# Performance work log

Measured on AMD Instinct MI355X. Metric: run time of the kernel, lower is better.

The kernel has to match this reference:

```python
import jax, jax.numpy as jnp
import numpy as np

N = 100000
E = 1_600_000
DIN = 24
DH = 64
DOUT = 12
NEG_SLOPE = 0.01  # torch F.leaky_relu default


def setup_inputs() -> dict:
    key = jax.random.key(0)
    ks = jax.random.split(key, 18)
    inp = {}
    inp["feats"] = jax.random.normal(ks[0], (N, DIN), dtype=jnp.float32)
    inp["e_w"] = jax.random.uniform(ks[1], (E, 1), dtype=jnp.float32)
    inp["snorm_n"] = jnp.ones((N, 1), dtype=jnp.float32)
    inp["snorm_e"] = jnp.ones((E, 1), dtype=jnp.float32)
    inp["src"] = jax.random.randint(ks[2], (E,), 0, N, dtype=jnp.int32)
    inp["dst"] = jax.random.randint(ks[3], (E,), 0, N, dtype=jnp.int32)
    s = 0.05
    inp["emb_h_W"] = jax.random.normal(ks[4], (DH, DIN), dtype=jnp.float32) * s
    inp["emb_h_b"] = jnp.zeros((DH,), dtype=jnp.float32)
    inp["emb_e_W"] = jax.random.normal(ks[5], (DH, 1), dtype=jnp.float32) * s
    inp["emb_e_b"] = jnp.zeros((DH,), dtype=jnp.float32)
    inp["W_self1"] = jax.random.normal(ks[6], (DH, DH), dtype=jnp.float32) * s
    inp["W_func1"] = jax.random.normal(ks[7], (DH, DH), dtype=jnp.float32) * s
    inp["attn1"] = jax.random.normal(ks[8], (3 * DH,), dtype=jnp.float32) * s
    inp["W_self2"] = jax.random.normal(ks[9], (DH, DH), dtype=jnp.float32) * s
    inp["W_func2"] = jax.random.normal(ks[10], (DH, DH), dtype=jnp.float32) * s
    inp["attn2"] = jax.random.normal(ks[11], (3 * DH,), dtype=jnp.float32) * s
    inp["lin1_W"] = jax.random.normal(ks[12], (DOUT, DH), dtype=jnp.float32) * s
    inp["lin1_b"] = jnp.zeros((DOUT,), dtype=jnp.float32)
    return inp


def _gat_layer(h, w_edge, src, dst, W_self, W_func, attn):
    # h: [N, d], w_edge: [E, d] edge embedding, attn: [3d]
    h_s = h @ W_self.T                       # linear_self(h)
    z = h @ W_func.T                         # linear_func(h)
    d = z.shape[-1]
    a_src, a_dst, a_w = attn[:d], attn[d:2 * d], attn[2 * d:]
    # attention score: W_a . [z_src, z_dst, w]  (decomposed to avoid [E,3d] concat)
    s_node_src = z @ a_src                   # [N]
    s_node_dst = z @ a_dst                   # [N]
    e = s_node_src[src] + s_node_dst[dst] + w_edge @ a_w  # [E]
    e = jax.nn.leaky_relu(e, NEG_SLOPE)
    # segment softmax over incoming edges per destination node
    m = jax.ops.segment_max(e, dst, num_segments=h.shape[0])
    ex = jnp.exp(e - m[dst])
    denom = jax.ops.segment_sum(ex, dst, num_segments=h.shape[0])
    alpha = ex / denom[dst]                  # [E]
    msg = alpha[:, None] * z[src]            # [E, d]
    agg = jax.ops.segment_sum(msg, dst, num_segments=h.shape[0])  # [N, d]
    # DGL: nodes with no incoming edges keep their old 'h' (not h_s + agg)
    in_deg = jax.ops.segment_sum(jnp.ones_like(e), dst, num_segments=h.shape[0])
    h_mid = jnp.where((in_deg > 0)[:, None], h_s + agg, h)
    return h + jax.nn.relu(h_mid)            # relu then residual


def reference(feats, e_w, snorm_n, snorm_e, src, dst,
              emb_h_W, emb_h_b, emb_e_W, emb_e_b,
              W_self1, W_func1, attn1, W_self2, W_func2, attn2,
              lin1_W, lin1_b):
    feats = feats.reshape(feats.shape[0], -1)
    h = feats @ emb_h_W.T + emb_h_b          # [N, DH]
    e = e_w @ emb_e_W.T + emb_e_b            # [E, DH]
    h = _gat_layer(h, e, src, dst, W_self1, W_func1, attn1)
    h = _gat_layer(h, e, src, dst, W_self2, W_func2, attn2)
    y = h @ lin1_W.T + lin1_b                # [N, DOUT]
    return y
```

## Files before the change

kernel.cpp:

```cpp
#include <hip/hip_runtime.h>
#include <hip/hip_fp16.h>

#define N_NODES 100000
#define N_EDGES 1600000
#define DIN 24
#define DH 64
#define DOUT 12
#define NEG_SLOPE 0.01f
#define NG 64
#define EPG (N_EDGES / NG)
#define NS 7
#define SLICE_N 16384
#define NTOT (NG * N_NODES)
#define SCAN_BLK 4096
#define LDSW 72

#define NB_HIST (NS * NG)
#define NB_SUMDEG ((N_NODES + 255) / 256)
#define NB_SCAN1N ((N_NODES + SCAN_BLK - 1) / SCAN_BLK)
#define NB_SCAT ((N_EDGES + 255) / 256)
#define NB_NODE ((N_NODES + 63) / 64)
#define NB_NODE_T ((NB_NODE + 1) / 2)
#define NB_AGG ((N_NODES + 7) / 8)

typedef _Float16 half8_t __attribute__((ext_vector_type(8)));
typedef float floatx4 __attribute__((ext_vector_type(4)));

__device__ __forceinline__ void dev_consts(const float* emb_e_W, const float* emb_e_b,
                                           const float* attn1, const float* attn2,
                                           float* consts) {
    int lane = threadIdx.x;
    if (lane >= 64) return;
    float w = emb_e_W[lane], b = emb_e_b[lane];
    float a1 = attn1[2 * DH + lane], a2 = attn2[2 * DH + lane];
    float c11 = w * a1, c01 = b * a1, c12 = w * a2, c02 = b * a2;
    for (int off = 32; off; off >>= 1) {
        c11 += __shfl_down(c11, off);
        c01 += __shfl_down(c01, off);
        c12 += __shfl_down(c12, off);
        c02 += __shfl_down(c02, off);
    }
    if (lane == 0) {
        consts[0] = c11; consts[1] = c01; consts[2] = c12; consts[3] = c02;
    }
}

__device__ __forceinline__ void dev_hist(int bid, const int* dst,
                                         unsigned char* deg, unsigned char* rank) {
    __shared__ unsigned cnt[SLICE_N / 4];
    int s = bid % NS, c = bid / NS;
    for (int i = threadIdx.x; i < SLICE_N / 4; i += 1024) cnt[i] = 0;
    __syncthreads();
    int nbase = s * SLICE_N;
    int start = c * EPG, end = start + EPG;
    for (int i = start + threadIdx.x; i < end; i += 1024) {
        int local = dst[i] - nbase;
        if ((unsigned)local < SLICE_N) {
            unsigned sh = (unsigned)(local & 3) * 8u;
            unsigned old = atomicAdd(&cnt[local >> 2], 1u << sh);
            rank[i] = (unsigned char)((old >> sh) & 255u);
        }
    }
    __syncthreads();
    int nmax = N_NODES - nbase;
    if (nmax > SLICE_N) nmax = SLICE_N;
    unsigned* dw = (unsigned*)(deg + (size_t)c * N_NODES + nbase);
    for (int l = threadIdx.x; l < (nmax >> 2); l += 1024) dw[l] = cnt[l];
}

__device__ __forceinline__ void dev_scan1(int bid, const int* in, int* out,
                                          int* part, int n) {
    __shared__ int lds[256];
    int t = threadIdx.x;
    int base = bid * SCAN_BLK + t * 16;
    int v[16];
    int s = 0;
#pragma unroll
    for (int i = 0; i < 16; ++i) {
        int idx = base + i;
        v[i] = (idx < n) ? in[idx] : 0;
        s += v[i];
    }
    lds[t] = s;
    __syncthreads();
    for (int off = 1; off < 256; off <<= 1) {
        int y = (t >= off) ? lds[t - off] : 0;
        __syncthreads();
        lds[t] += y;
        __syncthreads();
    }
    int run = lds[t] - s;
#pragma unroll
    for (int i = 0; i < 16; ++i) {
        int idx = base + i;
        if (idx < n) out[idx] = run;
        run += v[i];
    }
    if (t == 255) part[bid] = lds[255];
}

__device__ __forceinline__ void dev_scan2(int* part, int nblk, int* row_offN) {
    __shared__ int lds2[256];
    int t = threadIdx.x;
    int v[4];
    int s = 0;
#pragma unroll
    for (int i = 0; i < 4; ++i) {
        int idx = t * 4 + i;
        v[i] = (idx < nblk) ? part[idx] : 0;
        s += v[i];
    }
    lds2[t] = s;
    __syncthreads();
    for (int off = 1; off < 256; off <<= 1) {
        int y = (t >= off) ? lds2[t - off] : 0;
        __syncthreads();
        lds2[t] += y;
        __syncthreads();
    }
    int run = lds2[t] - s;
#pragma unroll
    for (int i = 0; i < 4; ++i) {
        int idx = t * 4 + i;
        if (idx < nblk) part[idx] = run;
        run += v[i];
    }
    if (row_offN) {
        __syncthreads();
        if (t == 0) row_offN[N_NODES] = N_EDGES - part[N_NODES >> 12];
    }
}

__device__ __forceinline__ void dev_sumdeg(int bid, const unsigned char* degB,
                                           int* degN, unsigned char* chunkOff) {
    int n = bid * 256 + threadIdx.x;
    if (n >= N_NODES) return;
    int run = 0;
    for (int g = 0; g < NG; ++g) {
        size_t idx = (size_t)g * N_NODES + n;
        int v = (int)degB[idx];
        chunkOff[idx] = (unsigned char)run;
        run += v;
    }
    degN[n] = run;
}

__device__ __forceinline__ void dev_nodeME(int bid, int stride,
                                           const float* feats, const float* embW,
                                           const float* embB,
                                           const float* Wself, const float* Wfunc,
                                           const float* attn,
                                           __half* h16, __half* zh, __half* hs16,
                                           float* s_src, float* s_dst) {
    __shared__ _Float16 lds[2 * 64 * LDSW];
    __shared__ _Float16 wembH[64 * 40];
    __shared__ float biasS[64];
    __shared__ _Float16 hbufH[4][16 * 72];
    int tid = threadIdx.x;
    for (int idx = tid; idx < 2 * 64 * 64; idx += 256) {
        int mat = idx >> 12, rem = idx & 4095;
        int o = rem >> 6, k = rem & 63;
        float v = mat ? Wfunc[rem] : Wself[rem];
        lds[(mat * 64 + o) * LDSW + k] = (_Float16)v;
    }
    for (int idx = tid; idx < 64 * 32; idx += 256) {
        int o = idx >> 5, k = idx & 31;
        wembH[o * 40 + k] = (_Float16)((k < DIN) ? embW[o * DIN + k] : 0.f);
    }
    if (tid < 64) biasS[tid] = embB[tid];
    __syncthreads();

    int wave = tid >> 6, lane = tid & 63;
    int quad = lane >> 4, lm = lane & 15;
    float asv[4], adv[4];
#pragma unroll
    for (int t = 0; t < 4; ++t) {
        asv[t] = attn[t * 16 + lm];
        adv[t] = attn[DH + t * 16 + lm];
    }
    const _Float16* bS = lds;
    const _Float16* bF = lds + 64 * LDSW;
    _Float16* hb = hbufH[wave];

    for (int tb = bid; tb < NB_NODE; tb += stride) {
        int n0 = (tb * 4 + wave) * 16;
        if (n0 >= N_NODES) continue;

        half8_t afE;
#pragma unroll
        for (int j = 0; j < 8; ++j) afE[j] = (_Float16)0.f;
        if (quad < 3) {
            const float* f = feats + (size_t)(n0 + lm) * DIN + quad * 8;
            float4 q0 = *(const float4*)(f);
            float4 q1 = *(const float4*)(f + 4);
            afE[0] = (_Float16)q0.x; afE[1] = (_Float16)q0.y;
            afE[2] = (_Float16)q0.z; afE[3] = (_Float16)q0.w;
            afE[4] = (_Float16)q1.x; afE[5] = (_Float16)q1.y;
            afE[6] = (_Float16)q1.z; afE[7] = (_Float16)q1.w;
        }
        floatx4 accE[4];
#pragma unroll
        for (int t = 0; t < 4; ++t) accE[t] = (floatx4)0.f;
#pragma unroll
        for (int t = 0; t < 4; ++t) {
            int o = t * 16 + lm;
            half8_t bE = *(const half8_t*)(wembH + o * 40 + quad * 8);
            accE[t] = __builtin_amdgcn_mfma_f32_16x16x32_f16(afE, bE, accE[t], 0, 0, 0);
        }
#pragma unroll
        for (int t = 0; t < 4; ++t) {
            float bv = biasS[t * 16 + lm];
#pragma unroll
            for (int r = 0; r < 4; ++r) {
                float hv = accE[t][r] + bv;
                int node = n0 + quad * 4 + r;
                h16[(size_t)node * DH + t * 16 + lm] = __float2half(hv);
                hb[(quad * 4 + r) * 72 + t * 16 + lm] = (_Float16)hv;
            }
        }
        half8_t afrag[2];
#pragma unroll
        for (int ks = 0; ks < 2; ++ks)
            afrag[ks] = *(const half8_t*)(hb + lm * 72 + ks * 32 + quad * 8);

        floatx4 accS[4], accF[4];
#pragma unroll
        for (int t = 0; t < 4; ++t) { accS[t] = (floatx4)0.f; accF[t] = (floatx4)0.f; }
#pragma unroll
        for (int t = 0; t < 4; ++t) {
            int o = t * 16 + lm;
#pragma unroll
            for (int ks = 0; ks < 2; ++ks) {
                int hoff = o * LDSW + ks * 32 + quad * 8;
                half8_t b1 = *(const half8_t*)(bS + hoff);
                half8_t b2 = *(const half8_t*)(bF + hoff);
                accS[t] = __builtin_amdgcn_mfma_f32_16x16x32_f16(afrag[ks], b1, accS[t], 0, 0, 0);
                accF[t] = __builtin_amdgcn_mfma_f32_16x16x32_f16(afrag[ks], b2, accF[t], 0, 0, 0);
            }
        }

        float ps[4] = {0.f, 0.f, 0.f, 0.f}, pd[4] = {0.f, 0.f, 0.f, 0.f};
#pragma unroll
        for (int t = 0; t < 4; ++t) {
#pragma unroll
            for (int r = 0; r < 4; ++r) {
                int node = n0 + quad * 4 + r;
                float zv = accF[t][r];
                zh[(size_t)node * DH + t * 16 + lm] = __float2half(zv);
                hs16[(size_t)node * DH + t * 16 + lm] = __float2half(accS[t][r]);
                ps[r] += zv * asv[t];
                pd[r] += zv * adv[t];
            }
        }
#pragma unroll
        for (int r = 0; r < 4; ++r) {
            float p1 = ps[r], p2 = pd[r];
            for (int off = 8; off; off >>= 1) {
                p1 += __shfl_xor(p1, off);
                p2 += __shfl_xor(p2, off);
            }
            if (lm == 0) {
                s_src[n0 + quad * 4 + r] = p1;
                s_dst[n0 + quad * 4 + r] = p2;
            }
        }
    }
}

__device__ __forceinline__ void dev_nodeM(int bid, int stride, const __half* h16,
                                          const float* Wself, const float* Wfunc,
                                          const float* attn,
                                          __half* zh, __half* hs16,
                                          float* s_src, float* s_dst) {
    __shared__ _Float16 lds[2 * 64 * LDSW];
    int tid = threadIdx.x;
    for (int idx = tid; idx < 2 * 64 * 64; idx += 256) {
        int mat = idx >> 12, rem = idx & 4095;
        int o = rem >> 6, k = rem & 63;
        float v = mat ? Wfunc[rem] : Wself[rem];
        lds[(mat * 64 + o) * LDSW + k] = (_Float16)v;
    }
    __syncthreads();

    int wave = tid >> 6, lane = tid & 63;
    int quad = lane >> 4, lm = lane & 15;
    float asv[4], adv[4];
#pragma unroll
    for (int t = 0; t < 4; ++t) {
        asv[t] = attn[t * 16 + lm];
        adv[t] = attn[DH + t * 16 + lm];
    }
    const _Float16* bS = lds;
    const _Float16* bF = lds + 64 * LDSW;

    for (int tb = bid; tb < NB_NODE; tb += stride) {
        int n0 = (tb * 4 + wave) * 16;
        if (n0 >= N_NODES) continue;

        const _Float16* hrow = (const _Float16*)h16 + (size_t)(n0 + lm) * DH;
        half8_t afrag[2];
#pragma unroll
        for (int ks = 0; ks < 2; ++ks)
            afrag[ks] = *(const half8_t*)(hrow + ks * 32 + quad * 8);

        floatx4 accS[4], accF[4];
#pragma unroll
        for (int t = 0; t < 4; ++t) { accS[t] = (floatx4)0.f; accF[t] = (floatx4)0.f; }

#pragma unroll
        for (int t = 0; t < 4; ++t) {
            int o = t * 16 + lm;
#pragma unroll
            for (int ks = 0; ks < 2; ++ks) {
                int hoff = o * LDSW + ks * 32 + quad * 8;
                half8_t b1 = *(const half8_t*)(bS + hoff);
                half8_t b2 = *(const half8_t*)(bF + hoff);
                accS[t] = __builtin_amdgcn_mfma_f32_16x16x32_f16(afrag[ks], b1, accS[t], 0, 0, 0);
                accF[t] = __builtin_amdgcn_mfma_f32_16x16x32_f16(afrag[ks], b2, accF[t], 0, 0, 0);
            }
        }

        float ps[4] = {0.f, 0.f, 0.f, 0.f}, pd[4] = {0.f, 0.f, 0.f, 0.f};
#pragma unroll
        for (int t = 0; t < 4; ++t) {
#pragma unroll
            for (int r = 0; r < 4; ++r) {
                int node = n0 + quad * 4 + r;
                float zv = accF[t][r];
                zh[(size_t)node * DH + t * 16 + lm] = __float2half(zv);
                hs16[(size_t)node * DH + t * 16 + lm] = __float2half(accS[t][r]);
                ps[r] += zv * asv[t];
                pd[r] += zv * adv[t];
            }
        }
#pragma unroll
        for (int r = 0; r < 4; ++r) {
            float p1 = ps[r], p2 = pd[r];
            for (int off = 8; off; off >>= 1) {
                p1 += __shfl_xor(p1, off);
                p2 += __shfl_xor(p2, off);
            }
            if (lm == 0) {
                s_src[n0 + quad * 4 + r] = p1;
                s_dst[n0 + quad * 4 + r] = p2;
            }
        }
    }
}

__global__ void __launch_bounds__(1024, 2)
k_fuse1(const int* __restrict__ dst, unsigned char* __restrict__ deg,
        unsigned char* __restrict__ rank,
        const float* __restrict__ emb_e_W, const float* __restrict__ emb_e_b,
        const float* __restrict__ attn1, const float* __restrict__ attn2,
        float* __restrict__ consts) {
    int bid = blockIdx.x;
    if (bid == 0) { dev_consts(emb_e_W, emb_e_b, attn1, attn2, consts); return; }
    dev_hist(bid - 1, dst, deg, rank);
}

__global__ void __launch_bounds__(256, 4)
k_fuse2(const unsigned char* __restrict__ degB, int* __restrict__ degN,
        unsigned char* __restrict__ chunkOff,
        const float* __restrict__ feats, const float* __restrict__ embW,
        const float* __restrict__ embB,
        __half* __restrict__ h16, const float* __restrict__ Wself1,
        const float* __restrict__ Wfunc1, const float* __restrict__ attn1,
        __half* __restrict__ zh, __half* __restrict__ hs16,
        float* __restrict__ s_src, float* __restrict__ s_dst) {
    int bid = blockIdx.x;
    if (bid < NB_NODE_T) {
        dev_nodeME(bid, NB_NODE_T, feats, embW, embB, Wself1, Wfunc1, attn1,
                   h16, zh, hs16, s_src, s_dst);
        return;
    }
    dev_sumdeg(bid - NB_NODE_T, degB, degN, chunkOff);
}

__global__ void k_prep3(const int* __restrict__ degN, int* __restrict__ row_offN,
                        int* __restrict__ partN) {
    dev_scan1(blockIdx.x, degN, row_offN, partN, N_NODES);
}

__global__ void k_prep4(int* __restrict__ partN, int* __restrict__ row_offN) {
    dev_scan2(partN, NB_SCAN1N, row_offN);
}

__global__ void __launch_bounds__(256, 8)
k_scat(const int* __restrict__ src, const int* __restrict__ dst,
       const float* __restrict__ e_w, const unsigned char* __restrict__ rank,
       const int* __restrict__ row_offN, const int* __restrict__ partN,
       const unsigned char* __restrict__ chunkOff, unsigned* __restrict__ csr2) {
    int i = blockIdx.x * 256 + threadIdx.x;
    if (i >= N_EDGES) return;
    int g = i / EPG;
    int d = dst[i];
    unsigned qv = (unsigned)(e_w[i] * 32768.f);
    if (qv > 32767u) qv = 32767u;
    unsigned w = (unsigned)src[i] | (qv << 17);
    int pos = row_offN[d] + partN[d >> 12] + (int)chunkOff[(size_t)g * N_NODES + d]
            + (int)rank[i];
    csr2[pos] = w;
}

__global__ void __launch_bounds__(256, 4)
k_nodeL(const __half* __restrict__ h16, const float* __restrict__ Wself,
        const float* __restrict__ Wfunc, const float* __restrict__ attn,
        __half* __restrict__ zh, __half* __restrict__ hs16,
        float* __restrict__ s_src, float* __restrict__ s_dst) {
    dev_nodeM(blockIdx.x, NB_NODE_T, h16, Wself, Wfunc, attn, zh, hs16, s_src, s_dst);
}

__global__ void k_agg(const int* __restrict__ row_off, const int* __restrict__ partN,
                      const unsigned* __restrict__ csr,
                      const float* __restrict__ s_src, const float* __restrict__ s_dstA,
                      const float* __restrict__ consts, int layer,
                      const __half* __restrict__ zh, const __half* __restrict__ hsb,
                      __half* __restrict__ h16,
                      const float* __restrict__ lin_W, const float* __restrict__ lin_b,
                      float* __restrict__ y, int final_layer) {
    int wave = threadIdx.x >> 6, lane = threadIdx.x & 63;
    int half = lane >> 5, hl = lane & 31;
    int eg = (lane >> 3) & 3, c8 = lane & 7;
    int n = blockIdx.x * 8 + wave * 2 + half;
    if (n >= N_NODES) return;
    int rs = row_off[n] + partN[n >> 12];
    int re = row_off[n + 1] + partN[(n + 1) >> 12];
    int deg = re - rs;
    int degO = __shfl_xor(deg, 32);
    int degmax = deg > degO ? deg : degO;

    float c1 = consts[layer * 2 + 0];
    float c0 = consts[layer * 2 + 1];
    float sd = s_dstA[n];

    float acc[8];
#pragma unroll
    for (int k = 0; k < 8; ++k) acc[k] = 0.f;
    float ssl = 0.f;
    int lbase = lane & 32;

    for (int base = 0; base < degmax; base += 32) {
        float ex = 0.f;
        int s0 = 0;
        int idx = base + hl;
        if (idx < deg) {
            unsigned w = csr[rs + idx];
            s0 = (int)(w & 0x1FFFFu);
            float ew = (float)(w >> 17) * (1.f / 32768.f);
            float e = s_src[s0] + sd + ew * c1 + c0;
            e = (e > 0.f) ? e : NEG_SLOPE * e;
            ex = __expf(e);
        }
        ssl += ex;
        int cnt = degmax - base;
        if (cnt > 32) cnt = 32;
#pragma unroll 4
        for (int jb = 0; jb < cnt; jb += 4) {
            int srcl = lbase + jb + eg;
            int sj = __shfl(s0, srcl);
            float exj = __shfl(ex, srcl);
            half8_t zv = *(const half8_t*)((const _Float16*)zh + ((size_t)sj << 6) + (c8 << 3));
#pragma unroll
            for (int k = 0; k < 8; ++k) acc[k] += exj * (float)zv[k];
        }
    }
#pragma unroll
    for (int k = 0; k < 8; ++k) {
        acc[k] += __shfl_xor(acc[k], 8);
        acc[k] += __shfl_xor(acc[k], 16);
    }
    ssl += __shfl_xor(ssl, 16); ssl += __shfl_xor(ssl, 8);
    ssl += __shfl_xor(ssl, 4);  ssl += __shfl_xor(ssl, 2);
    ssl += __shfl_xor(ssl, 1);

    half8_t hv8 = *(const half8_t*)((const _Float16*)h16 + (size_t)n * DH + (c8 << 3));
    float hold[8];
#pragma unroll
    for (int k = 0; k < 8; ++k) hold[k] = (float)hv8[k];
    float hnew[8];
    if (deg == 0) {
#pragma unroll
        for (int k = 0; k < 8; ++k) hnew[k] = hold[k] + fmaxf(hold[k], 0.f);
    } else {
        float rinv = 1.f / ssl;
        half8_t hs8 = *(const half8_t*)((const _Float16*)hsb + (size_t)n * DH + (c8 << 3));
#pragma unroll
        for (int k = 0; k < 8; ++k)
            hnew[k] = hold[k] + fmaxf((float)hs8[k] + acc[k] * rinv, 0.f);
    }

    if (!final_layer) {
        if (eg == 0) {
            half8_t o8;
#pragma unroll
            for (int k = 0; k < 8; ++k) o8[k] = (_Float16)hnew[k];
            *(half8_t*)((_Float16*)h16 + (size_t)n * DH + (c8 << 3)) = o8;
        }
    } else {
#pragma unroll
        for (int t = 0; t < 3; ++t) {
            int o = eg * 3 + t;
            const float* wr = lin_W + o * DH + c8 * 8;
            float p = 0.f;
#pragma unroll
            for (int k = 0; k < 8; ++k) p += hnew[k] * wr[k];
            p += __shfl_xor(p, 1); p += __shfl_xor(p, 2); p += __shfl_xor(p, 4);
            if (c8 == 0) y[n * DOUT + o] = p + lin_b[o];
        }
    }
}

extern "C" void kernel_launch(void* const* d_in, const int* in_sizes, int n_in,
                              void* d_out, int out_size, void* d_ws, size_t ws_size,
                              hipStream_t stream) {
    const float* feats   = (const float*)d_in[0];
    const float* e_w     = (const float*)d_in[1];
    const int*   src     = (const int*)d_in[4];
    const int*   dst     = (const int*)d_in[5];
    const float* emb_h_W = (const float*)d_in[6];
    const float* emb_h_b = (const float*)d_in[7];
    const float* emb_e_W = (const float*)d_in[8];
    const float* emb_e_b = (const float*)d_in[9];
    const float* Wself[2] = {(const float*)d_in[10], (const float*)d_in[13]};
    const float* Wfunc[2] = {(const float*)d_in[11], (const float*)d_in[14]};
    const float* attn[2]  = {(const float*)d_in[12], (const float*)d_in[15]};
    const float* lin1_W  = (const float*)d_in[16];
    const float* lin1_b  = (const float*)d_in[17];
    float* y = (float*)d_out;

    char* ws = (char*)d_ws;
    size_t off = 0;
    auto alloc = [&](size_t bytes) {
        void* p = ws + off;
        off += (bytes + 255) & ~(size_t)255;
        return p;
    };
    __half*         h16      = (__half*)alloc((size_t)N_NODES * DH * 2);
    __half*         zh       = (__half*)alloc((size_t)N_NODES * DH * 2);
    __half*         hs16     = (__half*)alloc((size_t)N_NODES * DH * 2);
    unsigned*       csr2     = (unsigned*)alloc((size_t)N_EDGES * 4);
    float*          s_src    = (float*)alloc((size_t)N_NODES * 4);
    float*          s_dst    = (float*)alloc((size_t)N_NODES * 4);
    int*            row_offN = (int*)alloc((size_t)(N_NODES + 1) * 4);
    unsigned char*  deg      = (unsigned char*)alloc((size_t)NTOT + 256);
    unsigned char*  chunkOff = (unsigned char*)alloc((size_t)NTOT + 256);
    unsigned char*  rank     = (unsigned char*)alloc((size_t)N_EDGES);
    int*            degN     = (int*)alloc((size_t)N_NODES * 4);
    int*            partN    = (int*)alloc(1024 * 4);
    float*          consts   = (float*)alloc(4 * 4);

    k_fuse1<<<1 + NB_HIST, 1024, 0, stream>>>(dst, deg, rank, emb_e_W, emb_e_b,
                                              attn[0], attn[1], consts);
    k_fuse2<<<NB_NODE_T + NB_SUMDEG, 256, 0, stream>>>(
        deg, degN, chunkOff, feats, emb_h_W, emb_h_b,
        h16, Wself[0], Wfunc[0], attn[0], zh, hs16, s_src, s_dst);
    k_prep3<<<NB_SCAN1N, 256, 0, stream>>>(degN, row_offN, partN);
    k_prep4<<<1, 256, 0, stream>>>(partN, row_offN);
    k_scat<<<NB_SCAT, 256, 0, stream>>>(src, dst, e_w, rank, row_offN, partN,
                                        chunkOff, csr2);
    k_agg<<<NB_AGG, 256, 0, stream>>>(row_offN, partN, csr2, s_src, s_dst, consts, 0,
                                      zh, hs16, h16, lin1_W, lin1_b, y, 0);
    k_nodeL<<<NB_NODE_T, 256, 0, stream>>>(h16, Wself[1], Wfunc[1], attn[1],
                                           zh, hs16, s_src, s_dst);
    k_agg<<<NB_AGG, 256, 0, stream>>>(row_offN, partN, csr2, s_src, s_dst, consts, 1,
                                      zh, hs16, h16, lin1_W, lin1_b, y, 1);
}
```

Measured before the change: 278.6 us.

## Compute attention scores per edge-group lane instead of shuffling from a score phase

```diff
diff --git a/kernel.cpp b/kernel.cpp
--- a/kernel.cpp
+++ b/kernel.cpp
@@ -411,80 +411,69 @@
     dev_nodeM(blockIdx.x, NB_NODE_T, h16, Wself, Wfunc, attn, zh, hs16, s_src, s_dst);
 }
 
-__global__ void k_agg(const int* __restrict__ row_off, const int* __restrict__ partN,
-                      const unsigned* __restrict__ csr,
-                      const float* __restrict__ s_src, const float* __restrict__ s_dstA,
-                      const float* __restrict__ consts, int layer,
-                      const __half* __restrict__ zh, const __half* __restrict__ hsb,
-                      __half* __restrict__ h16,
-                      const float* __restrict__ lin_W, const float* __restrict__ lin_b,
-                      float* __restrict__ y, int final_layer) {
+__global__ void __launch_bounds__(256, 8)
+k_agg(const int* __restrict__ row_off, const int* __restrict__ partN,
+      const unsigned* __restrict__ csr,
+      const float* __restrict__ s_src, const float* __restrict__ s_dstA,
+      const float* __restrict__ consts, int layer,
+      const __half* __restrict__ zh, const __half* __restrict__ hsb,
+      __half* __restrict__ h16,
+      const float* __restrict__ lin_W, const float* __restrict__ lin_b,
+      float* __restrict__ y, int final_layer) {
     int wave = threadIdx.x >> 6, lane = threadIdx.x & 63;
-    int half = lane >> 5, hl = lane & 31;
+    int half = lane >> 5;
     int eg = (lane >> 3) & 3, c8 = lane & 7;
     int n = blockIdx.x * 8 + wave * 2 + half;
     if (n >= N_NODES) return;
     int rs = row_off[n] + partN[n >> 12];
     int re = row_off[n + 1] + partN[(n + 1) >> 12];
     int deg = re - rs;
-    int degO = __shfl_xor(deg, 32);
-    int degmax = deg > degO ? deg : degO;
 
     float c1 = consts[layer * 2 + 0];
     float c0 = consts[layer * 2 + 1];
     float sd = s_dstA[n];
 
-    float acc[8];
-#pragma unroll
-    for (int k = 0; k < 8; ++k) acc[k] = 0.f;
-    float ssl = 0.f;
-    int lbase = lane & 32;
-
-    for (int base = 0; base < degmax; base += 32) {
-        float ex = 0.f;
-        int s0 = 0;
-        int idx = base + hl;
-        if (idx < deg) {
-            unsigned w = csr[rs + idx];
-            s0 = (int)(w & 0x1FFFFu);
+    float hnew[8];
+    unsigned noff = ((unsigned)n << 7) | ((unsigned)c8 << 4);
+    half8_t hv8 = *(const half8_t*)((const char*)h16 + noff);
+    float hold[8];
+#pragma unroll
+    for (int k = 0; k < 8; ++k) hold[k] = (float)hv8[k];
+
+    if (deg == 0) {
+#pragma unroll
+        for (int k = 0; k < 8; ++k) hnew[k] = hold[k] + fmaxf(hold[k], 0.f);
+    } else {
+        float acc[8];
+#pragma unroll
+        for (int k = 0; k < 8; ++k) acc[k] = 0.f;
+        float ssl = 0.f;
+
+        for (int j0 = 0; j0 < deg; j0 += 4) {
+            int j = j0 + eg;
+            int jj = (j < deg) ? j : (deg - 1);
+            unsigned w = csr[rs + jj];
+            int s0 = (int)(w & 0x1FFFFu);
             float ew = (float)(w >> 17) * (1.f / 32768.f);
             float e = s_src[s0] + sd + ew * c1 + c0;
             e = (e > 0.f) ? e : NEG_SLOPE * e;
-            ex = __expf(e);
-        }
-        ssl += ex;
-        int cnt = degmax - base;
-        if (cnt > 32) cnt = 32;
-#pragma unroll 4
-        for (int jb = 0; jb < cnt; jb += 4) {
-            int srcl = lbase + jb + eg;
-            int sj = __shfl(s0, srcl);
-            float exj = __shfl(ex, srcl);
-            half8_t zv = *(const half8_t*)((const _Float16*)zh + ((size_t)sj << 6) + (c8 << 3));
-#pragma unroll
-            for (int k = 0; k < 8; ++k) acc[k] += exj * (float)zv[k];
-        }
-    }
-#pragma unroll
-    for (int k = 0; k < 8; ++k) {
-        acc[k] += __shfl_xor(acc[k], 8);
-        acc[k] += __shfl_xor(acc[k], 16);
-    }
-    ssl += __shfl_xor(ssl, 16); ssl += __shfl_xor(ssl, 8);
-    ssl += __shfl_xor(ssl, 4);  ssl += __shfl_xor(ssl, 2);
-    ssl += __shfl_xor(ssl, 1);
-
-    half8_t hv8 = *(const half8_t*)((const _Float16*)h16 + (size_t)n * DH + (c8 << 3));
-    float hold[8];
-#pragma unroll
-    for (int k = 0; k < 8; ++k) hold[k] = (float)hv8[k];
-    float hnew[8];
-    if (deg == 0) {
-#pragma unroll
-        for (int k = 0; k < 8; ++k) hnew[k] = hold[k] + fmaxf(hold[k], 0.f);
-    } else {
+            float ex = (j < deg) ? __expf(e) : 0.f;
+            ssl += ex;
+            unsigned boff = ((unsigned)s0 << 7) | ((unsigned)c8 << 4);
+            half8_t zv = *(const half8_t*)((const char*)zh + boff);
+#pragma unroll
+            for (int k = 0; k < 8; ++k) acc[k] += ex * (float)zv[k];
+        }
+#pragma unroll
+        for (int k = 0; k < 8; ++k) {
+            acc[k] += __shfl_xor(acc[k], 8);
+            acc[k] += __shfl_xor(acc[k], 16);
+        }
+        ssl += __shfl_xor(ssl, 8);
+        ssl += __shfl_xor(ssl, 16);
+
         float rinv = 1.f / ssl;
-        half8_t hs8 = *(const half8_t*)((const _Float16*)hsb + (size_t)n * DH + (c8 << 3));
+        half8_t hs8 = *(const half8_t*)((const char*)hsb + noff);
 #pragma unroll
         for (int k = 0; k < 8; ++k)
             hnew[k] = hold[k] + fmaxf((float)hs8[k] + acc[k] * rinv, 0.f);
@@ -495,7 +484,7 @@
             half8_t o8;
 #pragma unroll
             for (int k = 0; k < 8; ++k) o8[k] = (_Float16)hnew[k];
-            *(half8_t*)((_Float16*)h16 + (size_t)n * DH + (c8 << 3)) = o8;
+            *(half8_t*)((char*)h16 + noff) = o8;
         }
     } else {
 #pragma unroll
```

Measured after the change: 296.9 us. 6.6% more time.

## Fuse node embedding/matmul into histogram kernel and widen histogram slices

Applied to the files above, without the earlier changes.

```diff
diff --git a/kernel.cpp b/kernel.cpp
--- a/kernel.cpp
+++ b/kernel.cpp
@@ -9,8 +9,8 @@
 #define NEG_SLOPE 0.01f
 #define NG 64
 #define EPG (N_EDGES / NG)
-#define NS 7
-#define SLICE_N 16384
+#define NS 4
+#define SLICE_N 32768
 #define NTOT (NG * N_NODES)
 #define SCAN_BLK 4096
 #define LDSW 72
@@ -21,7 +21,13 @@
 #define NB_SCAT ((N_EDGES + 255) / 256)
 #define NB_NODE ((N_NODES + 63) / 64)
 #define NB_NODE_T ((NB_NODE + 1) / 2)
+#define NB_NME ((NB_NODE + 7) / 8)
 #define NB_AGG ((N_NODES + 7) / 8)
+
+#define SM_WEMB 18432
+#define SM_BIAS 23552
+#define SM_HBUF 23808
+#define SM_SIZE 60672
 
 typedef _Float16 half8_t __attribute__((ext_vector_type(8)));
 typedef float floatx4 __attribute__((ext_vector_type(4)));
@@ -45,9 +51,9 @@
     }
 }
 
-__device__ __forceinline__ void dev_hist(int bid, const int* dst,
+__device__ __forceinline__ void dev_hist(int bid, char* smem, const int* dst,
                                          unsigned char* deg, unsigned char* rank) {
-    __shared__ unsigned cnt[SLICE_N / 4];
+    unsigned* cnt = (unsigned*)smem;
     int s = bid % NS, c = bid / NS;
     for (int i = threadIdx.x; i < SLICE_N / 4; i += 1024) cnt[i] = 0;
     __syncthreads();
@@ -145,25 +151,25 @@
     degN[n] = run;
 }
 
-__device__ __forceinline__ void dev_nodeME(int bid, int stride,
+__device__ __forceinline__ void dev_nodeME(int bid, char* smem,
                                            const float* feats, const float* embW,
                                            const float* embB,
                                            const float* Wself, const float* Wfunc,
                                            const float* attn,
                                            __half* h16, __half* zh, __half* hs16,
                                            float* s_src, float* s_dst) {
-    __shared__ _Float16 lds[2 * 64 * LDSW];
-    __shared__ _Float16 wembH[64 * 40];
-    __shared__ float biasS[64];
-    __shared__ _Float16 hbufH[4][16 * 72];
+    _Float16* lds   = (_Float16*)smem;
+    _Float16* wembH = (_Float16*)(smem + SM_WEMB);
+    float*    biasS = (float*)(smem + SM_BIAS);
+    _Float16* hbufA = (_Float16*)(smem + SM_HBUF);
     int tid = threadIdx.x;
-    for (int idx = tid; idx < 2 * 64 * 64; idx += 256) {
+    for (int idx = tid; idx < 2 * 64 * 64; idx += 1024) {
         int mat = idx >> 12, rem = idx & 4095;
         int o = rem >> 6, k = rem & 63;
         float v = mat ? Wfunc[rem] : Wself[rem];
         lds[(mat * 64 + o) * LDSW + k] = (_Float16)v;
     }
-    for (int idx = tid; idx < 64 * 32; idx += 256) {
+    for (int idx = tid; idx < 64 * 32; idx += 1024) {
         int o = idx >> 5, k = idx & 31;
         wembH[o * 40 + k] = (_Float16)((k < DIN) ? embW[o * DIN + k] : 0.f);
     }
@@ -171,6 +177,7 @@
     __syncthreads();
 
     int wave = tid >> 6, lane = tid & 63;
+    int vb = wave >> 2, wv = wave & 3;
     int quad = lane >> 4, lm = lane & 15;
     float asv[4], adv[4];
 #pragma unroll
@@ -180,10 +187,10 @@
     }
     const _Float16* bS = lds;
     const _Float16* bF = lds + 64 * LDSW;
-    _Float16* hb = hbufH[wave];
-
-    for (int tb = bid; tb < NB_NODE; tb += stride) {
-        int n0 = (tb * 4 + wave) * 16;
+    _Float16* hb = hbufA + wave * (16 * 72);
+
+    for (int tb = bid * 4 + vb; tb < NB_NODE; tb += NB_NME * 4) {
+        int n0 = (tb * 4 + wv) * 16;
         if (n0 >= N_NODES) continue;
 
         half8_t afE;
@@ -353,28 +360,25 @@
         unsigned char* __restrict__ rank,
         const float* __restrict__ emb_e_W, const float* __restrict__ emb_e_b,
         const float* __restrict__ attn1, const float* __restrict__ attn2,
-        float* __restrict__ consts) {
-    int bid = blockIdx.x;
-    if (bid == 0) { dev_consts(emb_e_W, emb_e_b, attn1, attn2, consts); return; }
-    dev_hist(bid - 1, dst, deg, rank);
-}
-
-__global__ void __launch_bounds__(256, 4)
-k_fuse2(const unsigned char* __restrict__ degB, int* __restrict__ degN,
-        unsigned char* __restrict__ chunkOff,
+        float* __restrict__ consts,
         const float* __restrict__ feats, const float* __restrict__ embW,
         const float* __restrict__ embB,
         __half* __restrict__ h16, const float* __restrict__ Wself1,
-        const float* __restrict__ Wfunc1, const float* __restrict__ attn1,
+        const float* __restrict__ Wfunc1,
         __half* __restrict__ zh, __half* __restrict__ hs16,
         float* __restrict__ s_src, float* __restrict__ s_dst) {
+    __shared__ __align__(16) char smem[SM_SIZE];
     int bid = blockIdx.x;
-    if (bid < NB_NODE_T) {
-        dev_nodeME(bid, NB_NODE_T, feats, embW, embB, Wself1, Wfunc1, attn1,
-                   h16, zh, hs16, s_src, s_dst);
-        return;
-    }
-    dev_sumdeg(bid - NB_NODE_T, degB, degN, chunkOff);
+    if (bid == 0) { dev_consts(emb_e_W, emb_e_b, attn1, attn2, consts); return; }
+    bid -= 1;
+    if (bid < NB_HIST) { dev_hist(bid, smem, dst, deg, rank); return; }
+    dev_nodeME(bid - NB_HIST, smem, feats, embW, embB, Wself1, Wfunc1, attn1,
+               h16, zh, hs16, s_src, s_dst);
+}
+
+__global__ void k_prep2(const unsigned char* __restrict__ degB, int* __restrict__ degN,
+                        unsigned char* __restrict__ chunkOff) {
+    dev_sumdeg(blockIdx.x, degB, degN, chunkOff);
 }
 
 __global__ void k_prep3(const int* __restrict__ degN, int* __restrict__ row_offN,
@@ -460,7 +464,8 @@
             int srcl = lbase + jb + eg;
             int sj = __shfl(s0, srcl);
             float exj = __shfl(ex, srcl);
-            half8_t zv = *(const half8_t*)((const _Float16*)zh + ((size_t)sj << 6) + (c8 << 3));
+            unsigned boff = ((unsigned)sj << 7) | ((unsigned)c8 << 4);
+            half8_t zv = *(const half8_t*)((const char*)zh + boff);
 #pragma unroll
             for (int k = 0; k < 8; ++k) acc[k] += exj * (float)zv[k];
         }
@@ -474,7 +479,8 @@
     ssl += __shfl_xor(ssl, 4);  ssl += __shfl_xor(ssl, 2);
     ssl += __shfl_xor(ssl, 1);
 
-    half8_t hv8 = *(const half8_t*)((const _Float16*)h16 + (size_t)n * DH + (c8 << 3));
+    unsigned noff = ((unsigned)n << 7) | ((unsigned)c8 << 4);
+    half8_t hv8 = *(const half8_t*)((const char*)h16 + noff);
     float hold[8];
 #pragma unroll
     for (int k = 0; k < 8; ++k) hold[k] = (float)hv8[k];
@@ -484,7 +490,7 @@
         for (int k = 0; k < 8; ++k) hnew[k] = hold[k] + fmaxf(hold[k], 0.f);
     } else {
         float rinv = 1.f / ssl;
-        half8_t hs8 = *(const half8_t*)((const _Float16*)hsb + (size_t)n * DH + (c8 << 3));
+        half8_t hs8 = *(const half8_t*)((const char*)hsb + noff);
 #pragma unroll
         for (int k = 0; k < 8; ++k)
             hnew[k] = hold[k] + fmaxf((float)hs8[k] + acc[k] * rinv, 0.f);
@@ -495,7 +501,7 @@
             half8_t o8;
 #pragma unroll
             for (int k = 0; k < 8; ++k) o8[k] = (_Float16)hnew[k];
-            *(half8_t*)((_Float16*)h16 + (size_t)n * DH + (c8 << 3)) = o8;
+            *(half8_t*)((char*)h16 + noff) = o8;
         }
     } else {
 #pragma unroll
@@ -550,11 +556,10 @@
     int*            partN    = (int*)alloc(1024 * 4);
     float*          consts   = (float*)alloc(4 * 4);
 
-    k_fuse1<<<1 + NB_HIST, 1024, 0, stream>>>(dst, deg, rank, emb_e_W, emb_e_b,
-                                              attn[0], attn[1], consts);
-    k_fuse2<<<NB_NODE_T + NB_SUMDEG, 256, 0, stream>>>(
-        deg, degN, chunkOff, feats, emb_h_W, emb_h_b,
-        h16, Wself[0], Wfunc[0], attn[0], zh, hs16, s_src, s_dst);
+    k_fuse1<<<1 + NB_HIST + NB_NME, 1024, 0, stream>>>(
+        dst, deg, rank, emb_e_W, emb_e_b, attn[0], attn[1], consts,
+        feats, emb_h_W, emb_h_b, h16, Wself[0], Wfunc[0], zh, hs16, s_src, s_dst);
+    k_prep2<<<NB_SUMDEG, 256, 0, stream>>>(deg, degN, chunkOff);
     k_prep3<<<NB_SCAN1N, 256, 0, stream>>>(degN, row_offN, partN);
     k_prep4<<<1, 256, 0, stream>>>(partN, row_offN);
     k_scat<<<NB_SCAT, 256, 0, stream>>>(src, dst, e_w, rank, row_offN, partN,
```

Result: no change. 281.0 us (+0.9%).
